# Performance work log

Hardware: AMD Instinct MI355X
Metric: run time of the kernel (lower is better)

## Reference

```python
import jax, jax.numpy as jnp
import numpy as np

PAD = 4  # must match init_kwargs


def setup_inputs() -> dict:
    key = jax.random.key(0)
    k1, k2 = jax.random.split(key)
    n, c, h, w = 128, 9, 224, 224
    x = jax.random.normal(k1, (n, c, h, w), dtype=jnp.float32)
    # torch.randint(0, 2*pad+1, (n,1,1,2)) -> values in [0, 2*pad]
    shift = jax.random.randint(k2, (n, 1, 1, 2), 0, 2 * PAD + 1, dtype=jnp.int32)
    return {"x": x, "shift": shift}


def reference(x, shift):
    pad = PAD
    n, c, h, w = x.shape
    H2, W2 = h + 2 * pad, w + 2 * pad

    # replicate pad (torch F.pad mode='replicate' == jnp 'edge')
    xp = jnp.pad(x, ((0, 0), (0, 0), (pad, pad), (pad, pad)), mode='edge')
    xp = jnp.transpose(xp, (0, 2, 3, 1))  # (n, H2, W2, c) for batched gather

    eps_h = 1.0 / H2
    eps_w = 1.0 / W2
    ah = jnp.linspace(-1.0 + eps_h, 1.0 - eps_h, H2, dtype=x.dtype)[:h]  # (h,)
    aw = jnp.linspace(-1.0 + eps_w, 1.0 - eps_w, W2, dtype=x.dtype)[:w]  # (w,)
    # base_grid[..., 0] = x(width) coord, base_grid[..., 1] = y(height) coord
    base = jnp.stack(jnp.broadcast_arrays(aw[None, :], ah[:, None]), axis=-1)  # (h, w, 2)

    # shift *= 1/(h+2p) + 1/(w+2p)  (faithful to source, even if h != w)
    scale = jnp.asarray(1.0 / H2 + 1.0 / W2, dtype=x.dtype)
    grid = base[None] + shift.astype(x.dtype) * scale  # (n, h, w, 2)

    # grid_sample, bilinear, padding_mode='zeros', align_corners=False
    gx, gy = grid[..., 0], grid[..., 1]
    ix = ((gx + 1.0) * W2 - 1.0) * 0.5  # unnormalized pixel coords
    iy = ((gy + 1.0) * H2 - 1.0) * 0.5
    x0 = jnp.floor(ix)
    y0 = jnp.floor(iy)
    x1 = x0 + 1.0
    y1 = y0 + 1.0
    wx1 = ix - x0
    wx0 = 1.0 - wx1
    wy1 = iy - y0
    wy0 = 1.0 - wy1

    b = jnp.arange(n)[:, None, None]  # (n,1,1) batch index

    def corner(yi, xi):
        valid = ((xi >= 0) & (xi <= W2 - 1) & (yi >= 0) & (yi <= H2 - 1)).astype(x.dtype)
        xc = jnp.clip(xi, 0, W2 - 1).astype(jnp.int32)
        yc = jnp.clip(yi, 0, H2 - 1).astype(jnp.int32)
        return xp[b, yc, xc] * valid[..., None]  # (n, h, w, c)

    out = (corner(y0, x0) * (wy0 * wx0)[..., None]
           + corner(y0, x1) * (wy0 * wx1)[..., None]
           + corner(y1, x0) * (wy1 * wx0)[..., None]
           + corner(y1, x1) * (wy1 * wx1)[..., None])
    return jnp.transpose(out, (0, 3, 1, 2))  # (n, c, h, w)
```

## Files before the change

kernel.cpp:

```cpp
#include <hip/hip_runtime.h>


constexpr int PADC = 4;
constexpr int Nn = 128, Cc = 9, Hh = 224, Ww = 224;

__global__ __launch_bounds__(256) void shift_gather(
    const float* __restrict__ x, const int* __restrict__ shift,
    float* __restrict__ out)
{
    constexpr int W4          = Ww / 4;
    constexpr int vec_per_img = Cc * Hh * W4;
    const long total = (long)Nn * vec_per_img;

    long idx = (long)blockIdx.x * blockDim.x + threadIdx.x;
    if (idx >= total) return;

    int n   = (int)(idx / vec_per_img);
    int r   = (int)(idx - (long)n * vec_per_img);
    int chw = r / W4;
    int j4  = r - chw * W4;
    int i   = chw % Hh;

    int sx = shift[2 * n + 0] - PADC;
    int sy = shift[2 * n + 1] - PADC;

    int si = min(max(i + sy, 0), Hh - 1);

    const float* srow = x + ((long)n * Cc * Hh + (chw - i) + si) * (long)Ww;

    int j0 = 4 * j4;
    int jb = j0 + sx;
    float v0 = srow[min(max(jb    , 0), Ww - 1)];
    float v1 = srow[min(max(jb + 1, 0), Ww - 1)];
    float v2 = srow[min(max(jb + 2, 0), Ww - 1)];
    float v3 = srow[min(max(jb + 3, 0), Ww - 1)];

    float4 v = make_float4(v0, v1, v2, v3);
    *(float4*)(out + ((long)chw + (long)n * Cc * Hh) * Ww + j0) = v;
}

extern "C" void kernel_launch(void* const* d_in, const int* in_sizes, int n_in,
                              void* d_out, int out_size, void* d_ws, size_t ws_size,
                              hipStream_t stream) {
    const float* x     = (const float*)d_in[0];
    const int*   shift = (const int*)d_in[1];
    float*       out   = (float*)d_out;

    constexpr long total = (long)Nn * Cc * Hh * (Ww / 4);
    constexpr int  block = 256;
    const long grid = (total + block - 1) / block;

    hipLaunchKernelGGL(shift_gather, dim3((unsigned)grid), dim3(block), 0, stream,
                       x, shift, out);
}
```

Baseline: 380.0 us.

## Use 3D grid per row and single vector load with lane-select for shifted gather

Replaces the flat index decode (divisions and modulo) with a 3D grid where each wave handles one output row. The four clamped scalar loads become one possibly unaligned 4-wide vector load at a clamped offset, and the needed elements are chosen with selects. This reduces integer arithmetic and load instruction count. The cost is that 8 of 64 lanes per wave are idle, and misaligned vector loads may span cache lines.

```diff
diff --git a/kernel.cpp b/kernel.cpp
--- a/kernel.cpp
+++ b/kernel.cpp
@@ -4,39 +4,52 @@
 constexpr int PADC = 4;
 constexpr int Nn = 128, Cc = 9, Hh = 224, Ww = 224;
 
+typedef float f4u __attribute__((ext_vector_type(4), aligned(4)));
+typedef float f4a __attribute__((ext_vector_type(4)));
+
+__device__ __forceinline__ float pick4(f4a v, int s) {
+    float lo = (s & 1) ? v.y : v.x;
+    float hi = (s & 1) ? v.w : v.z;
+    return (s & 2) ? hi : lo;
+}
+
 __global__ __launch_bounds__(256) void shift_gather(
     const float* __restrict__ x, const int* __restrict__ shift,
     float* __restrict__ out)
 {
-    constexpr int W4          = Ww / 4;
-    constexpr int vec_per_img = Cc * Hh * W4;
-    const long total = (long)Nn * vec_per_img;
+    const int j4 = threadIdx.x & 63;
+    if (j4 >= Ww / 4) return;
+    const int wave = threadIdx.x >> 6;
+    const int i = blockIdx.x * 4 + wave;
+    const int c = blockIdx.y;
+    const int n = blockIdx.z;
 
-    long idx = (long)blockIdx.x * blockDim.x + threadIdx.x;
-    if (idx >= total) return;
+    const int sx = shift[2 * n + 0] - PADC;
+    const int sy = shift[2 * n + 1] - PADC;
 
-    int n   = (int)(idx / vec_per_img);
-    int r   = (int)(idx - (long)n * vec_per_img);
-    int chw = r / W4;
-    int j4  = r - chw * W4;
-    int i   = chw % Hh;
+    const int si = min(max(i + sy, 0), Hh - 1);
+    const long img = (long)(n * Cc + c) * Hh;
+    const float* __restrict__ srow = x + (img + si) * Ww;
 
-    int sx = shift[2 * n + 0] - PADC;
-    int sy = shift[2 * n + 1] - PADC;
+    const int j0  = j4 * 4;
+    const int jb  = j0 + sx;
+    const int jbc = min(max(jb, 0), Ww - 4);
 
-    int si = min(max(i + sy, 0), Hh - 1);
+    f4a v = *(const f4u*)(srow + jbc);
 
-    const float* srow = x + ((long)n * Cc * Hh + (chw - i) + si) * (long)Ww;
+    int s0 = min(max(jb + 0, 0), Ww - 1) - jbc;
+    int s1 = min(max(jb + 1, 0), Ww - 1) - jbc;
+    int s2 = min(max(jb + 2, 0), Ww - 1) - jbc;
+    int s3 = min(max(jb + 3, 0), Ww - 1) - jbc;
 
-    int j0 = 4 * j4;
-    int jb = j0 + sx;
-    float v0 = srow[min(max(jb    , 0), Ww - 1)];
-    float v1 = srow[min(max(jb + 1, 0), Ww - 1)];
-    float v2 = srow[min(max(jb + 2, 0), Ww - 1)];
-    float v3 = srow[min(max(jb + 3, 0), Ww - 1)];
+    f4a o;
+    o.x = pick4(v, s0);
+    o.y = pick4(v, s1);
+    o.z = pick4(v, s2);
+    o.w = pick4(v, s3);
 
-    float4 v = make_float4(v0, v1, v2, v3);
-    *(float4*)(out + ((long)chw + (long)n * Cc * Hh) * Ww + j0) = v;
+    float* drow = out + (img + i) * Ww;
+    *(f4a*)(drow + j0) = o;
 }
 
 extern "C" void kernel_launch(void* const* d_in, const int* in_sizes, int n_in,
@@ -46,10 +59,7 @@
     const int*   shift = (const int*)d_in[1];
     float*       out   = (float*)d_out;
 
-    constexpr long total = (long)Nn * Cc * Hh * (Ww / 4);
-    constexpr int  block = 256;
-    const long grid = (total + block - 1) / block;
-
-    hipLaunchKernelGGL(shift_gather, dim3((unsigned)grid), dim3(block), 0, stream,
-                       x, shift, out);
+    dim3 grid(Hh / 4, Cc, Nn);
+    dim3 block(256);
+    hipLaunchKernelGGL(shift_gather, grid, block, 0, stream, x, shift, out);
 }
```

New measurement: 374.4 us. Within noise of the previous version (-1.5%).
